# Performance work log

Hardware: AMD Instinct MI355X
Metric: run time of the kernel (lower is better)

## Reference

```python
import jax, jax.numpy as jnp
import numpy as np

NUM_CLASSES = 21
IOU_THR = 0.5
SCORE_THR = 0.04


def _conv(x, w, b, stride):
    # NCHW / OIHW, SAME padding
    y = jax.lax.conv_general_dilated(
        x, w, (stride, stride), 'SAME',
        dimension_numbers=('NCHW', 'OIHW', 'NCHW'))
    return y + b[None, :, None, None]


def _pairwise_iou(boxes):
    # original module which feeds locs straight into ops.nms.
    x1, y1, x2, y2 = boxes[:, 0], boxes[:, 1], boxes[:, 2], boxes[:, 3]
    area = (x2 - x1) * (y2 - y1)
    lt_x = jnp.maximum(x1[:, None], x1[None, :])
    lt_y = jnp.maximum(y1[:, None], y1[None, :])
    rb_x = jnp.minimum(x2[:, None], x2[None, :])
    rb_y = jnp.minimum(y2[:, None], y2[None, :])
    inter = jnp.clip(rb_x - lt_x, 0.0) * jnp.clip(rb_y - lt_y, 0.0)
    union = area[:, None] + area[None, :] - inter
    return inter / (union + 1e-9)


def _nms_keep(boxes, scores, valid):
    # Greedy NMS over score-sorted candidates; padded/masked, jit-friendly.
    order = jnp.argsort(-scores)
    b = boxes[order]            # [N,4]
    v = valid[order]            # [N]
    iou = _pairwise_iou(b)      # [N,N]
    n = boxes.shape[0]

    def body(i, keep):
        suppressed = jnp.any(keep & (iou[i] > IOU_THR))
        return keep.at[i].set(v[i] & jnp.logical_not(suppressed))

    keep = jax.lax.fori_loop(0, n, body, jnp.zeros((n,), bool))
    return order, keep


def _ssd_forward(x, bb_w1, bb_b1, bb_w2, bb_b2, bb_w3, bb_b3,
                 ex_w, ex_b, reg_w, reg_b, cls_w, cls_b):
    # backbone: three stride-2 conv+relu blocks
    h = jax.nn.relu(_conv(x, bb_w1, bb_b1, 2))
    h = jax.nn.relu(_conv(h, bb_w2, bb_b2, 2))
    h = jax.nn.relu(_conv(h, bb_w3, bb_b3, 2))
    # extras: one stride-2 conv+relu
    h = jax.nn.relu(_conv(h, ex_w, ex_b, 2))
    # heads
    locs = _conv(h, reg_w, reg_b, 1)    # [B, 4, H, W]
    confs = _conv(h, cls_w, cls_b, 1)   # [B, C, H, W]
    B = locs.shape[0]
    locs = jnp.transpose(locs, (0, 2, 3, 1)).reshape(B, -1, 4)        # [B, N, 4]
    confs = jnp.transpose(confs, (0, 2, 3, 1)).reshape(B, -1, NUM_CLASSES)  # [B, N, C]

    # PostProcessor: softmax -> max -> threshold mask -> NMS, vectorized over batch
    probs = jax.nn.softmax(confs, axis=-1)
    scores = jnp.max(probs, axis=-1)      # [B, N]
    labels = jnp.argmax(probs, axis=-1)   # [B, N]
    valid = scores > SCORE_THR

    order, keep = jax.vmap(_nms_keep)(locs, scores, valid)  # [B,N], [B,N] bool

    # The original's buggy inner loop leaves only the LAST image's results.
    i = B - 1
    o, k = order[i], keep[i]
    b_s = locs[i][o]
    s_s = scores[i][o]
    l_s = labels[i][o]
    c_s = confs[i][o]
    out_boxes = jnp.where(k[:, None], b_s, -1.0)
    out_labels = jnp.where(k, l_s, 0).astype(jnp.int64)
    out_scores = jnp.where(k, s_s, -1.0)
    out_confs = jnp.where(k[:, None], c_s, -1.0)
    return out_boxes, out_labels, out_scores, out_confs


def setup_inputs() -> dict:
    key = jax.random.key(0)
    ks = jax.random.split(key, 8)

    def w(k, shape):
        fan_in = shape[1] * shape[2] * shape[3]
        return jax.random.normal(k, shape, jnp.float32) / np.sqrt(fan_in)

    x = jax.random.normal(ks[0], (8, 3, 512, 512), jnp.float32)
    return {
        'x': x,
        'bb_w1': w(ks[1], (64, 3, 3, 3)),   'bb_b1': jnp.zeros((64,), jnp.float32),
        'bb_w2': w(ks[2], (128, 64, 3, 3)), 'bb_b2': jnp.zeros((128,), jnp.float32),
        'bb_w3': w(ks[3], (256, 128, 3, 3)),'bb_b3': jnp.zeros((256,), jnp.float32),
        'ex_w':  w(ks[4], (256, 256, 3, 3)),'ex_b':  jnp.zeros((256,), jnp.float32),
        'reg_w': w(ks[5], (4, 256, 3, 3)),  'reg_b': jnp.zeros((4,), jnp.float32),
        'cls_w': w(ks[6], (NUM_CLASSES, 256, 3, 3)), 'cls_b': jnp.zeros((NUM_CLASSES,), jnp.float32),
    }


def reference(x, bb_w1, bb_b1, bb_w2, bb_b2, bb_w3, bb_b3,
              ex_w, ex_b, reg_w, reg_b, cls_w, cls_b):
    return _ssd_forward(x, bb_w1, bb_b1, bb_w2, bb_b2, bb_w3, bb_b3,
                        ex_w, ex_b, reg_w, reg_b, cls_w, cls_b)
```

## Files before the change

### kernel.cpp

```cpp
#include <hip/hip_runtime.h>
#include <cstdint>
#include <cstddef>


__global__ __launch_bounds__(256) void k_repack_all(
    const float* __restrict__ w2, const float* __restrict__ w3,
    const float* __restrict__ w4, const float* __restrict__ regw,
    const float* __restrict__ clsw, float* __restrict__ wr2,
    float* __restrict__ wr3, float* __restrict__ wr4, float* __restrict__ wh) {
  int idx = blockIdx.x * 256 + threadIdx.x;
  if (idx < 73728) {
    int co = idx % 128, r = idx / 128, ci = r / 9, tap = r % 9;
    wr2[idx] = w2[(co * 64 + ci) * 9 + tap];
  } else if (idx < 73728 + 294912) {
    int i = idx - 73728;
    int co = i % 256, r = i / 256, ci = r / 9, tap = r % 9;
    wr3[i] = w3[(co * 128 + ci) * 9 + tap];
  } else if (idx < 73728 + 294912 + 589824) {
    int i = idx - (73728 + 294912);
    int co = i % 256, r = i / 256, ci = r / 9, tap = r % 9;
    wr4[i] = w4[(co * 256 + ci) * 9 + tap];
  } else if (idx < 73728 + 294912 + 589824 + 57600) {
    int i = idx - (73728 + 294912 + 589824);
    int ci = i & 255, r = i >> 8, tap = r / 25, o = r % 25;
    wh[i] = (o < 4) ? regw[(o * 256 + ci) * 9 + tap]
                    : clsw[((o - 4) * 256 + ci) * 9 + tap];
  }
}

__global__ __launch_bounds__(256) void k_conv1(const float* __restrict__ x,
                                               const float* __restrict__ w,
                                               const float* __restrict__ b,
                                               float* __restrict__ out) {
  __shared__ float in_t[3][33][33];
  const int tx = threadIdx.x, ty = threadIdx.y;
  const int tid = ty * 16 + tx;
  const int ox0 = blockIdx.x * 16, oy0 = blockIdx.y * 16;
  const int co0 = blockIdx.z * 16;
  for (int idx = tid; idx < 3 * 33 * 33; idx += 256) {
    int ci = idx / 1089, rem = idx % 1089;
    int r = rem / 33, c = rem % 33;
    int iy = oy0 * 2 + r, ix = ox0 * 2 + c;
    float v = 0.f;
    if (iy < 512 && ix < 512) v = x[(size_t)ci * 262144 + iy * 512 + ix];
    in_t[ci][r][c] = v;
  }
  __syncthreads();
  float rin[27];
#pragma unroll
  for (int ci = 0; ci < 3; ++ci)
#pragma unroll
    for (int kh = 0; kh < 3; ++kh)
#pragma unroll
      for (int kw = 0; kw < 3; ++kw)
        rin[ci * 9 + kh * 3 + kw] = in_t[ci][2 * ty + kh][2 * tx + kw];
  const int oy = oy0 + ty, ox = ox0 + tx;
  for (int co = co0; co < co0 + 16; ++co) {
    float a = 0.f;
#pragma unroll
    for (int k = 0; k < 27; ++k) a = fmaf(w[co * 27 + k], rin[k], a);
    out[(size_t)co * 65536 + oy * 256 + ox] = fmaxf(a + b[co], 0.f);
  }
}

template <int CIN, int COUT, int HIN, int WIN, int SH, int SW, int COPT,
          int CIT, int KSPLIT, int ROWW, int NW>
__global__ __launch_bounds__(NW * 64) void conv_s2(
    const float* __restrict__ in, const float* __restrict__ wr,
    const float* __restrict__ bias, float* __restrict__ out) {
  constexpr int HOUT = HIN / 2, WOUT = WIN / 2;
  constexpr int IH = SH * 2 + 1, IW = SW * 2 + 1;
  constexpr int EVW = SW + 1;
  constexpr int COT = NW * COPT;
  constexpr int NPAIR = CIT * IH * EVW;
  constexpr int NTHR = NW * 64;
  static_assert(SH * SW == 64, "one position per lane");
  static_assert(EVW + SW < ROWW + 1, "pad slot fits");
  __shared__ float lds[CIT * IH * ROWW];

  const int tid = threadIdx.x;
  const int gu  = __builtin_amdgcn_readfirstlane(tid >> 6);
  const int lp  = tid & 63;
  const int py  = lp / SW, px = lp % SW;

  constexpr int ntx = WOUT / SW;
  const int bx = blockIdx.x % ntx, by = blockIdx.x / ntx;
  const int ox0 = bx * SW, oy0 = by * SH;
  const int co_blk = blockIdx.y * COT;
  const int cobase = co_blk + gu * COPT;
  const int ci_begin = (KSPLIT > 1) ? blockIdx.z * (CIN / KSPLIT) : 0;
  constexpr int NST = (CIN / KSPLIT) / CIT;

  float acc[COPT] = {};

  for (int st = 0; st < NST; ++st) {
    const int cib = ci_begin + st * CIT;
    if (st) __syncthreads();
    for (int idx = tid; idx < NPAIR; idx += NTHR) {
      int ci = idx / (IH * EVW), rem = idx % (IH * EVW);
      int r = rem / EVW, c2 = rem % EVW;
      int iy = oy0 * 2 + r, ix = ox0 * 2 + 2 * c2;
      float v0 = 0.f, v1 = 0.f;
      const float* src = in + (size_t)(cib + ci) * HIN * WIN;
      if (iy < HIN) {
        if ((2 * c2 + 1 < IW) && (ix + 1 < WIN)) {
          float2 t = *(const float2*)(src + (size_t)iy * WIN + ix);
          v0 = t.x; v1 = t.y;
        } else if (ix < WIN) {
          v0 = src[(size_t)iy * WIN + ix];
        }
      }
      int rb = (ci * IH + r) * ROWW;
      lds[rb + c2] = v0;
      lds[rb + EVW + c2] = v1;
    }
    __syncthreads();
#pragma unroll 2
    for (int ci = 0; ci < CIT; ++ci) {
      const int b0 = (ci * IH + 2 * py) * ROWW + px;
      float e00 = lds[b0];
      float q0  = lds[b0 + EVW];
      float e01 = lds[b0 + 1];
      float e10 = lds[b0 + ROWW];
      float q1  = lds[b0 + ROWW + EVW];
      float e11 = lds[b0 + ROWW + 1];
      float e20 = lds[b0 + 2 * ROWW];
      float q2  = lds[b0 + 2 * ROWW + EVW];
      float e21 = lds[b0 + 2 * ROWW + 1];
      const float* wp = wr + (size_t)(cib + ci) * 9 * COUT + cobase;
#pragma unroll
      for (int c = 0; c < COPT; ++c) acc[c] = fmaf(e00, wp[c], acc[c]);
#pragma unroll
      for (int c = 0; c < COPT; ++c) acc[c] = fmaf(q0, wp[COUT + c], acc[c]);
#pragma unroll
      for (int c = 0; c < COPT; ++c) acc[c] = fmaf(e01, wp[2 * COUT + c], acc[c]);
#pragma unroll
      for (int c = 0; c < COPT; ++c) acc[c] = fmaf(e10, wp[3 * COUT + c], acc[c]);
#pragma unroll
      for (int c = 0; c < COPT; ++c) acc[c] = fmaf(q1, wp[4 * COUT + c], acc[c]);
#pragma unroll
      for (int c = 0; c < COPT; ++c) acc[c] = fmaf(e11, wp[5 * COUT + c], acc[c]);
#pragma unroll
      for (int c = 0; c < COPT; ++c) acc[c] = fmaf(e20, wp[6 * COUT + c], acc[c]);
#pragma unroll
      for (int c = 0; c < COPT; ++c) acc[c] = fmaf(q2, wp[7 * COUT + c], acc[c]);
#pragma unroll
      for (int c = 0; c < COPT; ++c) acc[c] = fmaf(e21, wp[8 * COUT + c], acc[c]);
    }
  }

  const int oy = oy0 + py, ox = ox0 + px;
#pragma unroll
  for (int c = 0; c < COPT; ++c) {
    int co = cobase + c;
    if constexpr (KSPLIT > 1) {
      out[((size_t)blockIdx.z * COUT + co) * (HOUT * WOUT) + oy * WOUT + ox] =
          acc[c];
    } else {
      out[(size_t)co * (HOUT * WOUT) + oy * WOUT + ox] =
          fmaxf(acc[c] + bias[co], 0.f);
    }
  }
}

__global__ __launch_bounds__(256) void k_combine(const float* __restrict__ part,
                                                 const float* __restrict__ b,
                                                 float* __restrict__ h4t) {
  int co = blockIdx.x;
  float bb = b[co];
  for (int k2 = 0; k2 < 4; ++k2) {
    int pos = threadIdx.x + k2 * 256;
    float v = part[(size_t)(0 * 256 + co) * 1024 + pos] +
              part[(size_t)(1 * 256 + co) * 1024 + pos] +
              part[(size_t)(2 * 256 + co) * 1024 + pos] +
              part[(size_t)(3 * 256 + co) * 1024 + pos];
    h4t[(size_t)pos * 256 + co] = fmaxf(v + bb, 0.f);
  }
}

__global__ __launch_bounds__(256) void k_head(const float* __restrict__ h4t,
                                              const float* __restrict__ wh,
                                              const float* __restrict__ regb,
                                              const float* __restrict__ clsb,
                                              float* __restrict__ locs,
                                              float* __restrict__ confs,
                                              float* __restrict__ scores,
                                              float* __restrict__ labelsF) {
  const int pos = blockIdx.x;
  const int py = pos >> 5, px = pos & 31;
  const int t = threadIdx.x;
  float part[25] = {};
#pragma unroll
  for (int kh = 0; kh < 3; ++kh) {
    int iy = py + kh - 1;
    if (iy < 0 || iy > 31) continue;
#pragma unroll
    for (int kw = 0; kw < 3; ++kw) {
      int ix = px + kw - 1;
      if (ix < 0 || ix > 31) continue;
      int tap = kh * 3 + kw;
      float v = h4t[(size_t)(iy * 32 + ix) * 256 + t];
      const float* wp = wh + (size_t)tap * 25 * 256 + t;
#pragma unroll
      for (int o = 0; o < 25; ++o)
        part[o] = fmaf(v, wp[(size_t)o * 256], part[o]);
    }
  }
#pragma unroll
  for (int o = 0; o < 25; ++o) {
#pragma unroll
    for (int d = 1; d < 64; d <<= 1) part[o] += __shfl_xor(part[o], d);
  }
  __shared__ float red[4][25];
  __shared__ float yv[25];
  const int wv = t >> 6, ln = t & 63;
  if (ln == 0) {
#pragma unroll
    for (int o = 0; o < 25; ++o) red[wv][o] = part[o];
  }
  __syncthreads();
  if (t < 25) {
    float y = red[0][t] + red[1][t] + red[2][t] + red[3][t];
    y += (t < 4) ? regb[t] : clsb[t - 4];
    if (t < 4) locs[(size_t)pos * 4 + t] = y;
    else       confs[(size_t)pos * 21 + (t - 4)] = y;
    yv[t] = y;
  }
  __syncthreads();
  if (t == 0) {
    float m = yv[4];
    int lab = 0;
    for (int j = 1; j < 21; ++j)
      if (yv[4 + j] > m) { m = yv[4 + j]; lab = j; }
    float s = 0.f;
    for (int j = 0; j < 21; ++j) s += expf(yv[4 + j] - m);
    scores[pos] = 1.f / s;
    labelsF[pos] = (float)lab;
  }
}

__global__ __launch_bounds__(512) void k_sort(const float* __restrict__ scores,
                                              const float* __restrict__ locs,
                                              int* __restrict__ order,
                                              float* __restrict__ ssc,
                                              float* __restrict__ bsrt,
                                              unsigned long long* __restrict__ vbits) {
  __shared__ float sk[1024];
  __shared__ int   si[1024];
  const int t = threadIdx.x;
  sk[t] = scores[t];           si[t] = t;
  sk[t + 512] = scores[t + 512]; si[t + 512] = t + 512;
  for (int k = 2; k <= 1024; k <<= 1) {
    for (int j = k >> 1; j > 0; j >>= 1) {
      __syncthreads();
      int i1 = ((t / j) * (2 * j)) + (t % j);
      int i2 = i1 + j;
      bool up = (i1 & k) == 0;
      float sa = sk[i1], sb = sk[i2];
      int ia = si[i1], ib = si[i2];
      bool b_before_a = (sb > sa) || (sb == sa && ib < ia);
      bool a_before_b = (sa > sb) || (sa == sb && ia < ib);
      bool sw = up ? b_before_a : a_before_b;
      if (sw) { sk[i1] = sb; sk[i2] = sa; si[i1] = ib; si[i2] = ia; }
    }
  }
  __syncthreads();
  for (int i = t; i < 1024; i += 512) {
    int oi = si[i];
    order[i] = oi;
    ssc[i] = sk[i];
    ((float4*)bsrt)[i] = ((const float4*)locs)[oi];
  }
  if (t < 16) {
    unsigned long long w = 0;
    for (int b2 = 0; b2 < 64; ++b2)
      if (sk[t * 64 + b2] > 0.04f) w |= (1ull << b2);
    vbits[t] = w;
  }
}

__global__ __launch_bounds__(256) void k_mask(const float* __restrict__ bsrt,
                                              unsigned long long* __restrict__ mask) {
  __shared__ float4 sb[1024];
  const int t = threadIdx.x;
  for (int idx = t; idx < 1024; idx += 256)
    sb[idx] = ((const float4*)bsrt)[idx];
  __syncthreads();
  const int i = blockIdx.x * 16 + (t & 15);
  const int w = t >> 4;
  float4 bi = sb[i];
  float ai = (bi.z - bi.x) * (bi.w - bi.y);
  unsigned long long bits = 0;
  for (int jj = 0; jj < 64; ++jj) {
    float4 bj = sb[w * 64 + jj];
    float aj = (bj.z - bj.x) * (bj.w - bj.y);
    float ltx = fmaxf(bi.x, bj.x), lty = fmaxf(bi.y, bj.y);
    float rbx = fminf(bi.z, bj.z), rby = fminf(bi.w, bj.w);
    float inter = fmaxf(rbx - ltx, 0.f) * fmaxf(rby - lty, 0.f);
    float uni = ai + aj - inter;
    float iou = inter / (uni + 1e-9f);
    if (iou > 0.5f) bits |= (1ull << jj);
  }
  mask[(size_t)i * 16 + w] = bits;
}

__global__ __launch_bounds__(1024) void k_nms_gather(
    const unsigned long long* __restrict__ mask,
    const unsigned long long* __restrict__ vbits,
    const int* __restrict__ order, const float* __restrict__ ssc,
    const float* __restrict__ locs, const float* __restrict__ confs,
    const float* __restrict__ labelsF, float* __restrict__ out) {
  __shared__ unsigned long long KEEP[16], DEAD[16];
  __shared__ int ncert;
  const int i = threadIdx.x;
  const int w = i >> 6, l = i & 63;

  unsigned long long R[16];
#pragma unroll
  for (int k = 0; k < 16; ++k) {
    unsigned long long m = 0;
    if (k < w) m = mask[(size_t)i * 16 + k];
    else if (k == w && l) m = mask[(size_t)i * 16 + k] & ((1ull << l) - 1ull);
    R[k] = m;
  }
  const bool valid = (vbits[w] >> l) & 1ull;

  if (i < 16) { KEEP[i] = 0ull; DEAD[i] = 0ull; }
  if (i == 0) ncert = 0;
  __syncthreads();

  int status = 0;
  for (;;) {
    unsigned long long s = 0, p = 0;
    if (status == 0) {
#pragma unroll
      for (int k = 0; k < 16; ++k) {
        unsigned long long K_ = KEEP[k], D_ = DEAD[k];
        s |= R[k] & K_;
        p |= R[k] & ~D_;
      }
    }
    __syncthreads();
    bool newKeep = false, newDead = false;
    if (status == 0) {
      if (!valid)      { status = 2; newDead = true; }
      else if (s)      { status = 2; newDead = true; }
      else if (!p)     { status = 1; newKeep = true; }
    }
    unsigned long long bk = __ballot(newKeep);
    unsigned long long bd = __ballot(newDead);
    if (l == 0) {
      if (bk) KEEP[w] |= bk;
      if (bd) DEAD[w] |= bd;
      int n = __popcll(bk) + __popcll(bd);
      if (n) atomicAdd(&ncert, n);
    }
    __syncthreads();
    if (ncert >= 1024) break;
  }

  const bool kp = (status == 1);
  const int oi = order[i];
  float4 bx = kp ? ((const float4*)locs)[oi]
                 : make_float4(-1.f, -1.f, -1.f, -1.f);
  ((float4*)out)[i] = bx;
  out[4096 + i] = kp ? labelsF[oi] : 0.f;
  out[5120 + i] = kp ? ssc[i] : -1.f;
  float* oc = out + 6144 + (size_t)i * 21;
  const float* cc = confs + (size_t)oi * 21;
#pragma unroll
  for (int c = 0; c < 21; ++c) oc[c] = kp ? cc[c] : -1.f;
}

extern "C" void kernel_launch(void* const* d_in, const int* in_sizes, int n_in,
                              void* d_out, int out_size, void* d_ws, size_t ws_size,
                              hipStream_t stream) {
  const float* x    = (const float*)d_in[0] + (size_t)7 * 3 * 512 * 512;
  const float* w1   = (const float*)d_in[1];
  const float* b1   = (const float*)d_in[2];
  const float* w2   = (const float*)d_in[3];
  const float* b2   = (const float*)d_in[4];
  const float* w3   = (const float*)d_in[5];
  const float* b3   = (const float*)d_in[6];
  const float* w4   = (const float*)d_in[7];
  const float* b4   = (const float*)d_in[8];
  const float* regw = (const float*)d_in[9];
  const float* regb = (const float*)d_in[10];
  const float* clsw = (const float*)d_in[11];
  const float* clsb = (const float*)d_in[12];
  float* out = (float*)d_out;
  char* ws = (char*)d_ws;

  float* h1    = (float*)(ws + 0);
  float* part4 = (float*)(ws + 0);
  float* h4t   = (float*)(ws + 9437184);
  float* h2    = (float*)(ws + 16777216);
  float* h3    = (float*)(ws + 25165824);
  float* wr2   = (float*)(ws + 29360128);
  float* wr3   = (float*)(ws + 29655040);
  float* wr4   = (float*)(ws + 30834688);
  float* wh    = (float*)(ws + 33193984);
  float* locs  = (float*)(ws + 33424384);
  float* confs = (float*)(ws + 33440768);
  float* scores  = (float*)(ws + 33526784);
  float* labelsF = (float*)(ws + 33530880);
  int*   order   = (int*)  (ws + 33534976);
  float* ssc     = (float*)(ws + 33539072);
  float* bsrt    = (float*)(ws + 33543168);
  unsigned long long* mask  = (unsigned long long*)(ws + 33559552);
  unsigned long long* vbits = (unsigned long long*)(ws + 33690624);

  k_repack_all<<<3969, 256, 0, stream>>>(w2, w3, w4, regw, clsw,
                                         wr2, wr3, wr4, wh);

  k_conv1<<<dim3(16, 16, 4), dim3(16, 16), 0, stream>>>(x, w1, b1, h1);

  conv_s2<64, 128, 256, 256, 4, 16, 8, 16, 1, 36, 4>
      <<<dim3(256, 4, 1), 256, 0, stream>>>(h1, wr2, b2, h2);
  conv_s2<128, 256, 128, 128, 8, 8, 4, 16, 1, 20, 4>
      <<<dim3(64, 16, 1), 256, 0, stream>>>(h2, wr3, b3, h3);
  conv_s2<256, 256, 64, 64, 8, 8, 4, 16, 4, 20, 4>
      <<<dim3(16, 16, 4), 256, 0, stream>>>(h3, wr4, (const float*)nullptr, part4);
  k_combine<<<256, 256, 0, stream>>>(part4, b4, h4t);

  k_head<<<1024, 256, 0, stream>>>(h4t, wh, regb, clsb, locs, confs, scores, labelsF);

  k_sort<<<1, 512, 0, stream>>>(scores, locs, order, ssc, bsrt, vbits);
  k_mask<<<64, 256, 0, stream>>>(bsrt, mask);
  k_nms_gather<<<1, 1024, 0, stream>>>(mask, vbits, order, ssc, locs, confs,
                                       labelsF, out);
}
```

Measured before the change: 398.6 us.

## Prefetch next input-channel tile into registers in strided conv, widen conv1 grid

The strided conv kernel now precomputes per-thread global and LDS offsets once. It also software-pipelines the input staging: the next channel tile's global loads are issued into registers before the compute on the current tile, which should hide global memory latency behind the FMAs. Launch bounds now request 4 waves per SIMD, which constrains register use and risks spills given the extra prefetch registers. Separately, conv1 computes 8 output channels per block over twice as many blocks, adding parallelism at the cost of staging the input tile twice as often.

```diff
diff --git a/kernel.cpp b/kernel.cpp
--- a/kernel.cpp
+++ b/kernel.cpp
@@ -36,7 +36,7 @@
   const int tx = threadIdx.x, ty = threadIdx.y;
   const int tid = ty * 16 + tx;
   const int ox0 = blockIdx.x * 16, oy0 = blockIdx.y * 16;
-  const int co0 = blockIdx.z * 16;
+  const int co0 = blockIdx.z * 8;
   for (int idx = tid; idx < 3 * 33 * 33; idx += 256) {
     int ci = idx / 1089, rem = idx % 1089;
     int r = rem / 33, c = rem % 33;
@@ -55,7 +55,7 @@
       for (int kw = 0; kw < 3; ++kw)
         rin[ci * 9 + kh * 3 + kw] = in_t[ci][2 * ty + kh][2 * tx + kw];
   const int oy = oy0 + ty, ox = ox0 + tx;
-  for (int co = co0; co < co0 + 16; ++co) {
+  for (int co = co0; co < co0 + 8; ++co) {
     float a = 0.f;
 #pragma unroll
     for (int k = 0; k < 27; ++k) a = fmaf(w[co * 27 + k], rin[k], a);
@@ -65,7 +65,7 @@
 
 template <int CIN, int COUT, int HIN, int WIN, int SH, int SW, int COPT,
           int CIT, int KSPLIT, int ROWW, int NW>
-__global__ __launch_bounds__(NW * 64) void conv_s2(
+__global__ __launch_bounds__(NW * 64, 4) void conv_s2(
     const float* __restrict__ in, const float* __restrict__ wr,
     const float* __restrict__ bias, float* __restrict__ out) {
   constexpr int HOUT = HIN / 2, WOUT = WIN / 2;
@@ -74,6 +74,7 @@
   constexpr int COT = NW * COPT;
   constexpr int NPAIR = CIT * IH * EVW;
   constexpr int NTHR = NW * 64;
+  constexpr int NLD = (NPAIR + NTHR - 1) / NTHR;
   static_assert(SH * SW == 64, "one position per lane");
   static_assert(EVW + SW < ROWW + 1, "pad slot fits");
   __shared__ float lds[CIT * IH * ROWW];
@@ -91,28 +92,56 @@
   const int ci_begin = (KSPLIT > 1) ? blockIdx.z * (CIN / KSPLIT) : 0;
   constexpr int NST = (CIN / KSPLIT) / CIT;
 
+  unsigned goff[NLD];
+  int      loff[NLD];
+  int      mode[NLD];
+#pragma unroll
+  for (int j = 0; j < NLD; ++j) {
+    int idx = tid + j * NTHR;
+    bool act = (idx < NPAIR);
+    int ci = idx / (IH * EVW), rem = idx % (IH * EVW);
+    int r = rem / EVW, c2 = rem % EVW;
+    int iy = oy0 * 2 + r, ix = ox0 * 2 + 2 * c2;
+    loff[j] = act ? (ci * IH + r) * ROWW + c2 : -1;
+    goff[j] = (unsigned)((ci_begin + ci) * HIN * WIN + iy * WIN + ix);
+    int m = 0;
+    if (act && iy < HIN) {
+      if ((2 * c2 + 1 < IW) && (ix + 1 < WIN)) m = 1;
+      else if (ix < WIN) m = 2;
+    }
+    mode[j] = m;
+  }
+
+  float2 pre[NLD];
+#pragma unroll
+  for (int j = 0; j < NLD; ++j) {
+    float2 t = make_float2(0.f, 0.f);
+    if (mode[j] == 1)      t = *(const float2*)(in + goff[j]);
+    else if (mode[j] == 2) t.x = in[goff[j]];
+    pre[j] = t;
+  }
+
   float acc[COPT] = {};
 
-  for (int st = 0; st < NST; ++st) {
+  unsigned adv = (unsigned)(CIT * HIN * WIN);
+  for (int st = 0; st < NST; ++st, adv += (unsigned)(CIT * HIN * WIN)) {
     const int cib = ci_begin + st * CIT;
     if (st) __syncthreads();
-    for (int idx = tid; idx < NPAIR; idx += NTHR) {
-      int ci = idx / (IH * EVW), rem = idx % (IH * EVW);
-      int r = rem / EVW, c2 = rem % EVW;
-      int iy = oy0 * 2 + r, ix = ox0 * 2 + 2 * c2;
-      float v0 = 0.f, v1 = 0.f;
-      const float* src = in + (size_t)(cib + ci) * HIN * WIN;
-      if (iy < HIN) {
-        if ((2 * c2 + 1 < IW) && (ix + 1 < WIN)) {
-          float2 t = *(const float2*)(src + (size_t)iy * WIN + ix);
-          v0 = t.x; v1 = t.y;
-        } else if (ix < WIN) {
-          v0 = src[(size_t)iy * WIN + ix];
-        }
+#pragma unroll
+    for (int j = 0; j < NLD; ++j) {
+      if (loff[j] >= 0) {
+        lds[loff[j]] = pre[j].x;
+        lds[loff[j] + EVW] = pre[j].y;
       }
-      int rb = (ci * IH + r) * ROWW;
-      lds[rb + c2] = v0;
-      lds[rb + EVW + c2] = v1;
+    }
+    if (st + 1 < NST) {
+#pragma unroll
+      for (int j = 0; j < NLD; ++j) {
+        float2 t = make_float2(0.f, 0.f);
+        if (mode[j] == 1)      t = *(const float2*)(in + goff[j] + adv);
+        else if (mode[j] == 2) t.x = in[goff[j] + adv];
+        pre[j] = t;
+      }
     }
     __syncthreads();
 #pragma unroll 2
@@ -413,7 +442,7 @@
   k_repack_all<<<3969, 256, 0, stream>>>(w2, w3, w4, regw, clsw,
                                          wr2, wr3, wr4, wh);
 
-  k_conv1<<<dim3(16, 16, 4), dim3(16, 16), 0, stream>>>(x, w1, b1, h1);
+  k_conv1<<<dim3(16, 16, 8), dim3(16, 16), 0, stream>>>(x, w1, b1, h1);
 
   conv_s2<64, 128, 256, 256, 4, 16, 8, 16, 1, 36, 4>
       <<<dim3(256, 4, 1), 256, 0, stream>>>(h1, wr2, b2, h2);
```

Result: faster. 369.1 us (-7.4%).
